# Optimization experiments

Measured on AMD Instinct MI355X. Metric: run time of the kernel, lower is better.

## Reference

```python
import jax, jax.numpy as jnp
import numpy as np

N, E, F, H, EA = 50000, 500000, 2000, 128, 2
NUM_BOND_TYPES = 100
COORDS_RANGE = 10.0
NORM_FACTOR = 100.0


def setup_inputs() -> dict:
    key = jax.random.key(0)
    ks = jax.random.split(key, 20)

    def lin(k, i, o, gain=1.0):
        # xavier-uniform-ish init, stored as [in, out] so forward is x @ W + b
        lim = gain * np.sqrt(6.0 / (i + o))
        return jax.random.uniform(k, (i, o), jnp.float32, -lim, lim)

    inp = {
        "h_a": jax.random.normal(ks[0], (N, H), jnp.float32),
        "x_a": jax.random.normal(ks[1], (N, 3), jnp.float32),
        "e_a_idx": jax.random.randint(ks[2], (2, E), 0, N),
        "e_a_type": jax.random.randint(ks[3], (E,), 0, NUM_BOND_TYPES),
        "e_a_attr": jax.random.normal(ks[4], (E, EA), jnp.float32),
        "coord_diff_a": jax.random.normal(ks[5], (E, 3), jnp.float32),
        "h_f": jax.random.normal(ks[6], (F, H), jnp.float32),
        "x_f": jax.random.normal(ks[7], (F, 3), jnp.float32),
        "bm_mat": jax.random.normal(ks[8], (N, F), jnp.float32) / np.sqrt(F),
        # parameters
        "bond_emb": jax.random.normal(ks[9], (NUM_BOND_TYPES, H), jnp.float32),
        "aW1": lin(ks[10], 2 * H + EA + H, H), "ab1": jnp.zeros((H,), jnp.float32),
        "aW2": lin(ks[11], H, H), "ab2": jnp.zeros((H,), jnp.float32),
        "aW3": lin(ks[12], H, 1, gain=0.001),  # xavier gain=0.001, no bias
        "fW1": lin(ks[13], 2 * H + EA, H), "fb1": jnp.zeros((H,), jnp.float32),
        "fW2": lin(ks[14], H, H), "fb2": jnp.zeros((H,), jnp.float32),
        "fW3": lin(ks[15], H, 1, gain=0.001),
    }
    return inp


def reference(h_a, x_a, e_a_idx, e_a_type, e_a_attr, coord_diff_a, h_f, x_f, bm_mat,
              bond_emb, aW1, ab1, aW2, ab2, aW3, fW1, fb1, fW2, fb2, fW3):
    silu = jax.nn.silu
    row, col = e_a_idx[0], e_a_idx[1]

    be = bond_emb[e_a_type]                              # [E, H]
    coord_diff_f = x_a - bm_mat @ x_f                    # [N, 3]
    radial_f = jnp.sum(coord_diff_f ** 2, axis=1, keepdims=True)  # [N, 1]
    norm_f = jnp.sqrt(radial_f + 1e-8)
    coord_diff_f = coord_diff_f / (norm_f + 1.0)

    inp_atom = jnp.concatenate([h_a[row], h_a[col], e_a_attr, be], axis=1)        # [E, 3H+2]
    inp_frag = jnp.concatenate([h_a, bm_mat @ h_f, radial_f, radial_f], axis=1)   # [N, 2H+2]

    m_atom = silu(silu(inp_atom @ aW1 + ab1) @ aW2 + ab2) @ aW3  # [E, 1]
    m_frag = silu(silu(inp_frag @ fW1 + fb1) @ fW2 + fb2) @ fW3  # [N, 1]

    trans_atom = coord_diff_a * jnp.tanh(m_atom) * COORDS_RANGE  # [E, 3]
    trans_frag = coord_diff_f * jnp.tanh(m_frag) * COORDS_RANGE  # [N, 3]

    agg_atom = jax.ops.segment_sum(trans_atom, row, num_segments=x_a.shape[0]) / NORM_FACTOR
    return x_a + agg_atom + trans_frag
```

## Files before the change

kernel.cpp:

```cpp
#include <hip/hip_runtime.h>
#include <hip/hip_bf16.h>


typedef __attribute__((ext_vector_type(8))) short bfrag8;
typedef __attribute__((ext_vector_type(16))) float f32x16;
typedef __attribute__((ext_vector_type(4))) float f32x4v;

#define MFMA32(A, B, C) __builtin_amdgcn_mfma_f32_32x32x16_bf16((A), (B), (C), 0, 0, 0)

__device__ __forceinline__ f32x16 zero16() {
  f32x16 v;
#pragma unroll
  for (int i = 0; i < 16; ++i) v[i] = 0.0f;
  return v;
}

__device__ __forceinline__ unsigned short bf16bits(float x) {
  __hip_bfloat16 b = __float2bfloat16(x);
  unsigned short u;
  __builtin_memcpy(&u, &b, 2);
  return u;
}

__device__ __forceinline__ unsigned pk2(float lo, float hi) {
  return (unsigned)bf16bits(lo) | ((unsigned)bf16bits(hi) << 16);
}

__device__ __forceinline__ bfrag8 ldfrag(const unsigned short* p) {
  return *reinterpret_cast<const bfrag8*>(p);
}

__device__ __forceinline__ bfrag8 frag4(unsigned f0, unsigned f1, unsigned f2, unsigned f3) {
  union { unsigned u[4]; bfrag8 v; } q;
  q.u[0] = f0; q.u[1] = f1; q.u[2] = f2; q.u[3] = f3;
  return q.v;
}

__device__ __forceinline__ float silu_f(float x) { return x / (1.0f + __expf(-x)); }


__global__ void cvt_bf16_kernel(const float* __restrict__ src, unsigned short* __restrict__ dst, int n4) {
  int t = blockIdx.x * blockDim.x + threadIdx.x;
  if (t < n4) {
    f32x4v v = *reinterpret_cast<const f32x4v*>(src + 4 * (size_t)t);
    unsigned* d = reinterpret_cast<unsigned*>(dst + 4 * (size_t)t);
    d[0] = pk2(v[0], v[1]);
    d[1] = pk2(v[2], v[3]);
  }
}

__global__ void hfp_kernel(const float* __restrict__ h_f, const float* __restrict__ fW1,
                           float* __restrict__ hfp) {
  int f = blockIdx.x, n = threadIdx.x;
  float acc = 0.0f;
  for (int k = 0; k < 128; ++k) acc += h_f[(size_t)f * 128 + k] * fW1[(size_t)(128 + k) * 128 + n];
  hfp[(size_t)f * 128 + n] = acc;
}

__global__ void pack_wT_kernel(const float* __restrict__ W, unsigned short* __restrict__ dst,
                               int kcCount, int Krows) {
  int t = blockIdx.x * blockDim.x + threadIdx.x;
  int total = kcCount * 4 * 64 * 8;
  if (t >= total) return;
  int j = t & 7, l = (t >> 3) & 63, rem = t >> 9;
  int nt = rem & 3, kc = rem >> 2;
  int k = kc * 16 + ((l >> 5) << 3) + j;
  int n = nt * 32 + (l & 31);
  float v = (k < Krows) ? W[(size_t)k * 128 + n] : 0.0f;
  dst[t] = bf16bits(v);
}

__global__ void pack_w1e_kernel(const float* __restrict__ aW1, const float* __restrict__ ab1,
                                unsigned short* __restrict__ dst) {
  int t = blockIdx.x * blockDim.x + threadIdx.x;
  if (t >= 4 * 64 * 8) return;
  int j = t & 7, l = (t >> 3) & 63, nt = (t >> 9) & 3;
  int k = ((l >> 5) << 3) + j;
  int n = nt * 32 + (l & 31);
  float v = (k == 0) ? aW1[(size_t)256 * 128 + n]
          : (k == 1) ? aW1[(size_t)257 * 128 + n]
          : (k == 2) ? ab1[n] : 0.0f;
  dst[t] = bf16bits(v);
}

__global__ void pack_bmat_kernel(const float* __restrict__ hfp, const float* __restrict__ x_f,
                                 unsigned short* __restrict__ dst, int total) {
  int t = blockIdx.x * blockDim.x + threadIdx.x;
  if (t >= total) return;
  int j = t & 7, l = (t >> 3) & 63, rem = t >> 9;
  int nt = rem % 5, kc = rem / 5;
  int k = kc * 16 + ((l >> 5) << 3) + j;
  int n = nt * 32 + (l & 31);
  float v;
  if (n < 128) v = hfp[(size_t)k * 128 + n];
  else if (n < 131) v = x_f[(size_t)k * 3 + (n - 128)];
  else v = 0.0f;
  dst[t] = bf16bits(v);
}

__global__ __launch_bounds__(64) void k1_bm_gemm(
    const float* __restrict__ bm, const unsigned short* __restrict__ bmT,
    float* __restrict__ outT, int N, int F) {
  const int lane = threadIdx.x;
  const int h = lane >> 5;
  const int ln = lane & 31;
  const int m = blockIdx.x * 32 + ln;
  const int mc = (m < N) ? m : (N - 1);
  const float* bp = bm + (size_t)mc * F + h * 8;
  const int KC = F >> 4;

  f32x16 acc[5];
#pragma unroll
  for (int i = 0; i < 5; ++i) acc[i] = zero16();

  f32x4v x0 = *reinterpret_cast<const f32x4v*>(bp);
  f32x4v x1 = *reinterpret_cast<const f32x4v*>(bp + 4);
  for (int kc = 0; kc < KC; ++kc) {
    f32x4v c0 = x0, c1 = x1;
    if (kc + 1 < KC) {
      x0 = *reinterpret_cast<const f32x4v*>(bp + (size_t)(kc + 1) * 16);
      x1 = *reinterpret_cast<const f32x4v*>(bp + (size_t)(kc + 1) * 16 + 4);
    }
    bfrag8 b = frag4(pk2(c0[0], c0[1]), pk2(c0[2], c0[3]), pk2(c1[0], c1[1]), pk2(c1[2], c1[3]));
    const unsigned short* wp = bmT + ((size_t)kc * 5 * 64 + lane) * 8;
#pragma unroll
    for (int nt = 0; nt < 5; ++nt) acc[nt] = MFMA32(ldfrag(wp + nt * 512), b, acc[nt]);
  }
  if (m < N) {
#pragma unroll
    for (int nt = 0; nt < 5; ++nt)
#pragma unroll
      for (int r = 0; r < 16; ++r) {
        int n = nt * 32 + (r & 3) + 8 * (r >> 2) + 4 * h;
        if (n < 131) outT[(size_t)n * N + m] = acc[nt][r];
      }
  }
}

__global__ __launch_bounds__(256) void k2_frag(
    const float* __restrict__ x_a, const unsigned short* __restrict__ h_bf,
    const float* __restrict__ k1T,
    const unsigned short* __restrict__ fW1aT, const unsigned short* __restrict__ fW2T,
    const float* __restrict__ fW1, const float* __restrict__ fb1,
    const float* __restrict__ fb2, const float* __restrict__ fW3,
    float* __restrict__ out, int N) {
  const int lane = threadIdx.x & 63;
  const int wid = threadIdx.x >> 6;
  const int h = lane >> 5;
  const int ln = lane & 31;
  const int i = blockIdx.x * 128 + wid * 32 + ln;
  const bool valid = (i < N);
  const int ic = valid ? i : (N - 1);

  float cd[3];
  float radial = 0.0f;
#pragma unroll
  for (int c = 0; c < 3; ++c) {
    float v = x_a[3 * (size_t)ic + c] - k1T[(size_t)(128 + c) * N + ic];
    cd[c] = v;
    radial += v * v;
  }

  f32x16 acc[4];
#pragma unroll
  for (int q = 0; q < 4; ++q) acc[q] = zero16();
  const unsigned short* hp = h_bf + (size_t)ic * 128 + h * 8;
#pragma unroll
  for (int kc = 0; kc < 8; ++kc) {
    bfrag8 b = ldfrag(hp + kc * 16);
    const unsigned short* wp = fW1aT + ((size_t)(kc * 4) * 64 + lane) * 8;
#pragma unroll
    for (int nt = 0; nt < 4; ++nt) acc[nt] = MFMA32(ldfrag(wp + nt * 512), b, acc[nt]);
  }

  unsigned w[4][8];
#pragma unroll
  for (int nt = 0; nt < 4; ++nt)
#pragma unroll
    for (int p = 0; p < 8; ++p) {
      const int r0 = 2 * p;
      const int n0 = nt * 32 + (r0 & 3) + 8 * (r0 >> 2) + 4 * h;
      const int n1 = n0 + 1;
      float q0 = acc[nt][r0] + k1T[(size_t)n0 * N + ic]
               + radial * (fW1[(size_t)256 * 128 + n0] + fW1[(size_t)257 * 128 + n0]) + fb1[n0];
      float q1 = acc[nt][r0 + 1] + k1T[(size_t)n1 * N + ic]
               + radial * (fW1[(size_t)256 * 128 + n1] + fW1[(size_t)257 * 128 + n1]) + fb1[n1];
      w[nt][p] = pk2(silu_f(q0), silu_f(q1));
    }

  f32x16 acc2[4];
#pragma unroll
  for (int q = 0; q < 4; ++q) acc2[q] = zero16();
#pragma unroll
  for (int kc = 0; kc < 8; ++kc) {
    const int nt1 = kc >> 1, o = (kc & 1) * 4;
    unsigned a0 = w[nt1][o + 0], a1 = w[nt1][o + 1], a2 = w[nt1][o + 2], a3 = w[nt1][o + 3];
    unsigned s0 = (unsigned)__shfl_xor((int)a0, 32);
    unsigned s1 = (unsigned)__shfl_xor((int)a1, 32);
    unsigned s2 = (unsigned)__shfl_xor((int)a2, 32);
    unsigned s3 = (unsigned)__shfl_xor((int)a3, 32);
    bfrag8 b = frag4(h ? s2 : a0, h ? s3 : a1, h ? a2 : s0, h ? a3 : s1);
    const unsigned short* wp = fW2T + ((size_t)(kc * 4) * 64 + lane) * 8;
#pragma unroll
    for (int nt = 0; nt < 4; ++nt) acc2[nt] = MFMA32(ldfrag(wp + nt * 512), b, acc2[nt]);
  }

  float part = 0.0f;
#pragma unroll
  for (int nt = 0; nt < 4; ++nt)
#pragma unroll
    for (int r = 0; r < 16; ++r) {
      int n = nt * 32 + (r & 3) + 8 * (r >> 2) + 4 * h;
      part += silu_f(acc2[nt][r] + fb2[n]) * fW3[n];
    }
  float mv = part + __shfl_xor(part, 32);

  if (valid && h == 0) {
    float nrm = sqrtf(radial + 1e-8f);
    float s = tanhf(mv) * 10.0f / (nrm + 1.0f);
#pragma unroll
    for (int c = 0; c < 3; ++c)
      out[3 * (size_t)i + c] = x_a[3 * (size_t)i + c] + cd[c] * s;
  }
}

__global__ __launch_bounds__(256) void k3_atom(
    const unsigned short* __restrict__ h_bf,
    const unsigned short* __restrict__ bond_bf,
    const int* __restrict__ eidx, const int* __restrict__ etype,
    const float* __restrict__ eattr, const float* __restrict__ cda,
    const unsigned short* __restrict__ W1aT, const unsigned short* __restrict__ W1bT,
    const unsigned short* __restrict__ W1cT, const unsigned short* __restrict__ W1eT,
    const unsigned short* __restrict__ W2T,
    const float* __restrict__ ab2, const float* __restrict__ aW3,
    float* __restrict__ out, int E) {
  const int lane = threadIdx.x & 63;
  const int wid = threadIdx.x >> 6;
  const int h = lane >> 5;
  const int ln = lane & 31;
  const int e = blockIdx.x * 128 + wid * 32 + ln;
  const bool valid = (e < E);
  const int ec = valid ? e : (E - 1);
  const int row = eidx[ec];
  const int col = eidx[(size_t)E + ec];
  const int typ = etype[ec];
  const float e0 = eattr[2 * (size_t)ec];
  const float e1 = eattr[2 * (size_t)ec + 1];

  const unsigned short* hr = h_bf + (size_t)row * 128 + h * 8;
  const unsigned short* hc = h_bf + (size_t)col * 128 + h * 8;
  const unsigned short* bb = bond_bf + (size_t)typ * 128 + h * 8;

  f32x16 acc[4];
#pragma unroll
  for (int q = 0; q < 4; ++q) acc[q] = zero16();

#pragma unroll
  for (int kc = 0; kc < 8; ++kc) {
    bfrag8 b = ldfrag(hr + kc * 16);
    const unsigned short* wp = W1aT + ((size_t)(kc * 4) * 64 + lane) * 8;
#pragma unroll
    for (int nt = 0; nt < 4; ++nt) acc[nt] = MFMA32(ldfrag(wp + nt * 512), b, acc[nt]);
  }
#pragma unroll
  for (int kc = 0; kc < 8; ++kc) {
    bfrag8 b = ldfrag(hc + kc * 16);
    const unsigned short* wp = W1bT + ((size_t)(kc * 4) * 64 + lane) * 8;
#pragma unroll
    for (int nt = 0; nt < 4; ++nt) acc[nt] = MFMA32(ldfrag(wp + nt * 512), b, acc[nt]);
  }
#pragma unroll
  for (int kc = 0; kc < 8; ++kc) {
    bfrag8 b = ldfrag(bb + kc * 16);
    const unsigned short* wp = W1cT + ((size_t)(kc * 4) * 64 + lane) * 8;
#pragma unroll
    for (int nt = 0; nt < 4; ++nt) acc[nt] = MFMA32(ldfrag(wp + nt * 512), b, acc[nt]);
  }
  {
    unsigned u0 = h ? 0u : pk2(e0, e1);
    unsigned u1 = h ? 0u : 0x00003F80u;
    bfrag8 b = frag4(u0, u1, 0u, 0u);
    const unsigned short* wp = W1eT + (size_t)lane * 8;
#pragma unroll
    for (int nt = 0; nt < 4; ++nt) acc[nt] = MFMA32(ldfrag(wp + nt * 512), b, acc[nt]);
  }

  unsigned w[4][8];
#pragma unroll
  for (int nt = 0; nt < 4; ++nt)
#pragma unroll
    for (int p = 0; p < 8; ++p)
      w[nt][p] = pk2(silu_f(acc[nt][2 * p]), silu_f(acc[nt][2 * p + 1]));

  f32x16 acc2[4];
#pragma unroll
  for (int q = 0; q < 4; ++q) acc2[q] = zero16();
#pragma unroll
  for (int kc = 0; kc < 8; ++kc) {
    const int nt1 = kc >> 1, o = (kc & 1) * 4;
    unsigned a0 = w[nt1][o + 0], a1 = w[nt1][o + 1], a2 = w[nt1][o + 2], a3 = w[nt1][o + 3];
    unsigned s0 = (unsigned)__shfl_xor((int)a0, 32);
    unsigned s1 = (unsigned)__shfl_xor((int)a1, 32);
    unsigned s2 = (unsigned)__shfl_xor((int)a2, 32);
    unsigned s3 = (unsigned)__shfl_xor((int)a3, 32);
    bfrag8 b = frag4(h ? s2 : a0, h ? s3 : a1, h ? a2 : s0, h ? a3 : s1);
    const unsigned short* wp = W2T + ((size_t)(kc * 4) * 64 + lane) * 8;
#pragma unroll
    for (int nt = 0; nt < 4; ++nt) acc2[nt] = MFMA32(ldfrag(wp + nt * 512), b, acc2[nt]);
  }

  float part = 0.0f;
#pragma unroll
  for (int nt = 0; nt < 4; ++nt)
#pragma unroll
    for (int r = 0; r < 16; ++r) {
      int n = nt * 32 + (r & 3) + 8 * (r >> 2) + 4 * h;
      part += silu_f(acc2[nt][r] + ab2[n]) * aW3[n];
    }
  float mv = part + __shfl_xor(part, 32);

  if (valid) {
    float t = tanhf(mv) * 0.1f;
    if (h == 0) {
      atomicAdd(out + 3 * (size_t)row + 0, cda[3 * (size_t)ec + 0] * t);
      atomicAdd(out + 3 * (size_t)row + 1, cda[3 * (size_t)ec + 1] * t);
    } else {
      atomicAdd(out + 3 * (size_t)row + 2, cda[3 * (size_t)ec + 2] * t);
    }
  }
}


extern "C" void kernel_launch(void* const* d_in, const int* in_sizes, int n_in,
                              void* d_out, int out_size, void* d_ws, size_t ws_size,
                              hipStream_t stream) {
  const float* h_a    = (const float*)d_in[0];
  const float* x_a    = (const float*)d_in[1];
  const int*   e_idx  = (const int*)d_in[2];
  const int*   e_type = (const int*)d_in[3];
  const float* e_attr = (const float*)d_in[4];
  const float* cda    = (const float*)d_in[5];
  const float* h_f    = (const float*)d_in[6];
  const float* x_f    = (const float*)d_in[7];
  const float* bm     = (const float*)d_in[8];
  const float* bond   = (const float*)d_in[9];
  const float* aW1    = (const float*)d_in[10];
  const float* ab1    = (const float*)d_in[11];
  const float* aW2    = (const float*)d_in[12];
  const float* ab2    = (const float*)d_in[13];
  const float* aW3    = (const float*)d_in[14];
  const float* fW1    = (const float*)d_in[15];
  const float* fb1    = (const float*)d_in[16];
  const float* fW2    = (const float*)d_in[17];
  const float* fb2    = (const float*)d_in[18];
  const float* fW3    = (const float*)d_in[19];
  float* out = (float*)d_out;

  const int N  = in_sizes[0] / 128;
  const int E  = in_sizes[2] / 2;
  const int F  = in_sizes[6] / 128;
  const int NB = in_sizes[9] / 128;
  const int KC = F / 16;

  char* wsp = (char*)d_ws;
  size_t off = 0;
  auto alloc = [&](size_t bytes) -> char* {
    char* p = wsp + off;
    off += (bytes + 255) & ~(size_t)255;
    return p;
  };
  unsigned short* h_bf    = (unsigned short*)alloc((size_t)N * 128 * 2);
  unsigned short* bond_bf = (unsigned short*)alloc((size_t)NB * 128 * 2);
  float*          hfp     = (float*)alloc((size_t)F * 128 * 4);
  unsigned short* bmT     = (unsigned short*)alloc((size_t)KC * 5 * 64 * 8 * 2);
  unsigned short* W1aT    = (unsigned short*)alloc(8 * 4 * 64 * 8 * 2);
  unsigned short* W1bT    = (unsigned short*)alloc(8 * 4 * 64 * 8 * 2);
  unsigned short* W1cT    = (unsigned short*)alloc(8 * 4 * 64 * 8 * 2);
  unsigned short* W2T     = (unsigned short*)alloc(8 * 4 * 64 * 8 * 2);
  unsigned short* fW1aT   = (unsigned short*)alloc(8 * 4 * 64 * 8 * 2);
  unsigned short* fW2T    = (unsigned short*)alloc(8 * 4 * 64 * 8 * 2);
  unsigned short* W1eT    = (unsigned short*)alloc(1 * 4 * 64 * 8 * 2);
  float*          k1T     = (float*)alloc((size_t)131 * N * 4);

  {
    int n4 = N * 128 / 4;
    cvt_bf16_kernel<<<(n4 + 255) / 256, 256, 0, stream>>>(h_a, h_bf, n4);
  }
  {
    int n4 = NB * 128 / 4;
    cvt_bf16_kernel<<<(n4 + 255) / 256, 256, 0, stream>>>(bond, bond_bf, n4);
  }
  hfp_kernel<<<F, 128, 0, stream>>>(h_f, fW1, hfp);
  {
    int total = KC * 5 * 64 * 8;
    pack_bmat_kernel<<<(total + 255) / 256, 256, 0, stream>>>(hfp, x_f, bmT, total);
  }
  pack_wT_kernel<<<64, 256, 0, stream>>>(aW1,                 W1aT, 8, 128);
  pack_wT_kernel<<<64, 256, 0, stream>>>(aW1 + 128 * 128,     W1bT, 8, 128);
  pack_wT_kernel<<<64, 256, 0, stream>>>(aW1 + 258 * 128,     W1cT, 8, 128);
  pack_wT_kernel<<<64, 256, 0, stream>>>(aW2,                 W2T,  8, 128);
  pack_wT_kernel<<<64, 256, 0, stream>>>(fW1,                 fW1aT, 8, 128);
  pack_wT_kernel<<<64, 256, 0, stream>>>(fW2,                 fW2T, 8, 128);
  pack_w1e_kernel<<<8, 256, 0, stream>>>(aW1, ab1, W1eT);

  k1_bm_gemm<<<(N + 31) / 32, 64, 0, stream>>>(bm, bmT, k1T, N, F);
  k2_frag<<<(N + 127) / 128, 256, 0, stream>>>(x_a, h_bf, k1T, fW1aT, fW2T,
                                               fW1, fb1, fb2, fW3, out, N);
  k3_atom<<<(E + 127) / 128, 256, 0, stream>>>(h_bf, bond_bf, e_idx, e_type, e_attr, cda,
                                               W1aT, W1bT, W1cT, W1eT, W2T, ab2, aW3, out, E);
}
```

Before: 384.1 us.

## Merge prep kernels and run bm GEMM alongside edge MLP in one launch

Folds the bf16 conversion, hfp matmul, weight packing and aggregation-buffer zeroing into a single block-partitioned prep kernel. The bm GEMM and edge MLP now run as one grid, so the long-K GEMM blocks can overlap with edge blocks instead of running serially. Edge atomics now target a separate agg buffer that the node kernel adds into the output. The h_bf layout is changed so each half-wave reads 64 contiguous elements, and the GEMM uses 4-wave blocks with a two-stage prefetch. Costs are an extra N×3 buffer and launch bounds (256,2) that may limit registers for the edge path.

```diff
diff --git a/kernel.cpp b/kernel.cpp
--- a/kernel.cpp
+++ b/kernel.cpp
@@ -38,49 +38,101 @@
 
 __device__ __forceinline__ float silu_f(float x) { return x / (1.0f + __expf(-x)); }
 
-
-__global__ void cvt_bf16_kernel(const float* __restrict__ src, unsigned short* __restrict__ dst, int n4) {
-  int t = blockIdx.x * blockDim.x + threadIdx.x;
-  if (t < n4) {
-    f32x4v v = *reinterpret_cast<const f32x4v*>(src + 4 * (size_t)t);
-    unsigned* d = reinterpret_cast<unsigned*>(dst + 4 * (size_t)t);
-    d[0] = pk2(v[0], v[1]);
-    d[1] = pk2(v[2], v[3]);
-  }
-}
-
-__global__ void hfp_kernel(const float* __restrict__ h_f, const float* __restrict__ fW1,
-                           float* __restrict__ hfp) {
-  int f = blockIdx.x, n = threadIdx.x;
-  float acc = 0.0f;
-  for (int k = 0; k < 128; ++k) acc += h_f[(size_t)f * 128 + k] * fW1[(size_t)(128 + k) * 128 + n];
-  hfp[(size_t)f * 128 + n] = acc;
-}
-
-__global__ void pack_wT_kernel(const float* __restrict__ W, unsigned short* __restrict__ dst,
-                               int kcCount, int Krows) {
-  int t = blockIdx.x * blockDim.x + threadIdx.x;
-  int total = kcCount * 4 * 64 * 8;
-  if (t >= total) return;
-  int j = t & 7, l = (t >> 3) & 63, rem = t >> 9;
-  int nt = rem & 3, kc = rem >> 2;
-  int k = kc * 16 + ((l >> 5) << 3) + j;
-  int n = nt * 32 + (l & 31);
-  float v = (k < Krows) ? W[(size_t)k * 128 + n] : 0.0f;
-  dst[t] = bf16bits(v);
-}
-
-__global__ void pack_w1e_kernel(const float* __restrict__ aW1, const float* __restrict__ ab1,
-                                unsigned short* __restrict__ dst) {
-  int t = blockIdx.x * blockDim.x + threadIdx.x;
-  if (t >= 4 * 64 * 8) return;
-  int j = t & 7, l = (t >> 3) & 63, nt = (t >> 9) & 3;
-  int k = ((l >> 5) << 3) + j;
-  int n = nt * 32 + (l & 31);
-  float v = (k == 0) ? aW1[(size_t)256 * 128 + n]
-          : (k == 1) ? aW1[(size_t)257 * 128 + n]
-          : (k == 2) ? ab1[n] : 0.0f;
-  dst[t] = bf16bits(v);
+__global__ __launch_bounds__(256) void prep_kernel(
+    const float* __restrict__ h_a, const float* __restrict__ bond,
+    const float* __restrict__ h_f,
+    const float* __restrict__ aW1, const float* __restrict__ ab1,
+    const float* __restrict__ aW2,
+    const float* __restrict__ fW1, const float* __restrict__ fW2,
+    unsigned short* __restrict__ h_bf, unsigned short* __restrict__ bond_bf,
+    float* __restrict__ hfp,
+    unsigned short* __restrict__ W1aT, unsigned short* __restrict__ W1bT,
+    unsigned short* __restrict__ W1cT, unsigned short* __restrict__ W1eT,
+    unsigned short* __restrict__ W2T,
+    unsigned short* __restrict__ fW1aT, unsigned short* __restrict__ fW2T,
+    float* __restrict__ agg,
+    int N, int NB, int F) {
+  const int t = threadIdx.x;
+  int bid = blockIdx.x;
+  const int G_A = (N * 16 + 255) >> 8;
+  const int G_B = (NB * 16 + 255) >> 8;
+  const int G_H = (F + 1) >> 1;
+
+  if (bid < G_A + G_B) {
+    const float* src = (bid < G_A) ? h_a : bond;
+    unsigned short* dst = (bid < G_A) ? h_bf : bond_bf;
+    int rows = (bid < G_A) ? N : NB;
+    int idx = (bid < G_A ? bid : bid - G_A) * 256 + t;
+    if (idx < rows * 16) {
+      int row = idx >> 4, g = idx & 15;
+      int h = g & 1, kc = g >> 1;
+      const f32x4v* s = reinterpret_cast<const f32x4v*>(src + (size_t)row * 128 + g * 8);
+      f32x4v v0 = s[0], v1 = s[1];
+      unsigned* d = reinterpret_cast<unsigned*>(dst + (size_t)row * 128 + h * 64 + kc * 8);
+      d[0] = pk2(v0[0], v0[1]);
+      d[1] = pk2(v0[2], v0[3]);
+      d[2] = pk2(v1[0], v1[1]);
+      d[3] = pk2(v1[2], v1[3]);
+    }
+    return;
+  }
+  bid -= G_A + G_B;
+  if (bid < G_H) {
+    int f = bid * 2 + (t >> 7), n = t & 127;
+    if (f < F) {
+      float acc = 0.0f;
+#pragma unroll 8
+      for (int k = 0; k < 128; ++k)
+        acc += h_f[(size_t)f * 128 + k] * fW1[(size_t)(128 + k) * 128 + n];
+      hfp[(size_t)f * 128 + n] = acc;
+    }
+    return;
+  }
+  bid -= G_H;
+  if (bid < 6 * 64) {
+    int p = bid >> 6;
+    int tt = (bid & 63) * 256 + t;
+    int j = tt & 7, l = (tt >> 3) & 63, rem = tt >> 9;
+    int nt = rem & 3, kc = rem >> 2;
+    int k = kc * 16 + ((l >> 5) << 3) + j;
+    int n = nt * 32 + (l & 31);
+    const float* W;
+    unsigned short* D;
+    switch (p) {
+      case 0: W = aW1;             D = W1aT;  break;
+      case 1: W = aW1 + 128 * 128; D = W1bT;  break;
+      case 2: W = aW1 + 258 * 128; D = W1cT;  break;
+      case 3: W = aW2;             D = W2T;   break;
+      case 4: W = fW1;             D = fW1aT; break;
+      default: W = fW2;            D = fW2T;  break;
+    }
+    D[tt] = bf16bits(W[(size_t)k * 128 + n]);
+    return;
+  }
+  bid -= 6 * 64;
+  if (bid < 8) {
+    int tt = bid * 256 + t;
+    if (tt < 4 * 64 * 8) {
+      int j = tt & 7, l = (tt >> 3) & 63, nt = (tt >> 9) & 3;
+      int k = ((l >> 5) << 3) + j;
+      int n = nt * 32 + (l & 31);
+      float v = (k == 0) ? aW1[(size_t)256 * 128 + n]
+              : (k == 1) ? aW1[(size_t)257 * 128 + n]
+              : (k == 2) ? ab1[n] : 0.0f;
+      W1eT[tt] = bf16bits(v);
+    }
+    return;
+  }
+  bid -= 8;
+  {
+    int i4 = (bid * 256 + t) * 4;
+    if (i4 + 3 < N * 3) {
+      *reinterpret_cast<f32x4v*>(agg + i4) = f32x4v{0.f, 0.f, 0.f, 0.f};
+    } else {
+      for (int c = 0; c < 4; ++c)
+        if (i4 + c < N * 3) agg[i4 + c] = 0.0f;
+    }
+  }
 }
 
 __global__ void pack_bmat_kernel(const float* __restrict__ hfp, const float* __restrict__ x_f,
@@ -98,48 +150,155 @@
   dst[t] = bf16bits(v);
 }
 
-__global__ __launch_bounds__(64) void k1_bm_gemm(
+__global__ __launch_bounds__(256, 2) void fused_k1_k3(
     const float* __restrict__ bm, const unsigned short* __restrict__ bmT,
-    float* __restrict__ outT, int N, int F) {
-  const int lane = threadIdx.x;
+    float* __restrict__ k1T,
+    const unsigned short* __restrict__ h_bf, const unsigned short* __restrict__ bond_bf,
+    const int* __restrict__ eidx, const int* __restrict__ etype,
+    const float* __restrict__ eattr, const float* __restrict__ cda,
+    const unsigned short* __restrict__ W1aT, const unsigned short* __restrict__ W1bT,
+    const unsigned short* __restrict__ W1cT, const unsigned short* __restrict__ W1eT,
+    const unsigned short* __restrict__ W2T,
+    const float* __restrict__ ab2, const float* __restrict__ aW3,
+    float* __restrict__ agg,
+    int N, int F, int E, int G1) {
+  const int lane = threadIdx.x & 63;
+  const int wid = threadIdx.x >> 6;
   const int h = lane >> 5;
   const int ln = lane & 31;
-  const int m = blockIdx.x * 32 + ln;
-  const int mc = (m < N) ? m : (N - 1);
-  const float* bp = bm + (size_t)mc * F + h * 8;
-  const int KC = F >> 4;
-
-  f32x16 acc[5];
-#pragma unroll
-  for (int i = 0; i < 5; ++i) acc[i] = zero16();
-
-  f32x4v x0 = *reinterpret_cast<const f32x4v*>(bp);
-  f32x4v x1 = *reinterpret_cast<const f32x4v*>(bp + 4);
-  for (int kc = 0; kc < KC; ++kc) {
-    f32x4v c0 = x0, c1 = x1;
-    if (kc + 1 < KC) {
-      x0 = *reinterpret_cast<const f32x4v*>(bp + (size_t)(kc + 1) * 16);
-      x1 = *reinterpret_cast<const f32x4v*>(bp + (size_t)(kc + 1) * 16 + 4);
-    }
-    bfrag8 b = frag4(pk2(c0[0], c0[1]), pk2(c0[2], c0[3]), pk2(c1[0], c1[1]), pk2(c1[2], c1[3]));
-    const unsigned short* wp = bmT + ((size_t)kc * 5 * 64 + lane) * 8;
-#pragma unroll
-    for (int nt = 0; nt < 5; ++nt) acc[nt] = MFMA32(ldfrag(wp + nt * 512), b, acc[nt]);
-  }
-  if (m < N) {
-#pragma unroll
-    for (int nt = 0; nt < 5; ++nt)
-#pragma unroll
-      for (int r = 0; r < 16; ++r) {
-        int n = nt * 32 + (r & 3) + 8 * (r >> 2) + 4 * h;
-        if (n < 131) outT[(size_t)n * N + m] = acc[nt][r];
+
+  if ((int)blockIdx.x < G1) {
+    const int m = blockIdx.x * 128 + wid * 32 + ln;
+    const int mc = (m < N) ? m : (N - 1);
+    const float* bp = bm + (size_t)mc * F + h * 8;
+    const int KC = F >> 4;
+
+    f32x16 acc[5];
+#pragma unroll
+    for (int i = 0; i < 5; ++i) acc[i] = zero16();
+
+    f32x4v a0 = *reinterpret_cast<const f32x4v*>(bp);
+    f32x4v a1 = *reinterpret_cast<const f32x4v*>(bp + 4);
+    f32x4v b0 = *reinterpret_cast<const f32x4v*>(bp + 16);
+    f32x4v b1 = *reinterpret_cast<const f32x4v*>(bp + 20);
+    for (int kc = 0; kc < KC; ++kc) {
+      f32x4v c0 = a0, c1 = a1;
+      a0 = b0; a1 = b1;
+      if (kc + 2 < KC) {
+        b0 = *reinterpret_cast<const f32x4v*>(bp + (size_t)(kc + 2) * 16);
+        b1 = *reinterpret_cast<const f32x4v*>(bp + (size_t)(kc + 2) * 16 + 4);
       }
+      bfrag8 b = frag4(pk2(c0[0], c0[1]), pk2(c0[2], c0[3]), pk2(c1[0], c1[1]), pk2(c1[2], c1[3]));
+      const unsigned short* wp = bmT + ((size_t)kc * 5 * 64 + lane) * 8;
+#pragma unroll
+      for (int nt = 0; nt < 5; ++nt) acc[nt] = MFMA32(ldfrag(wp + nt * 512), b, acc[nt]);
+    }
+    if (m < N) {
+#pragma unroll
+      for (int nt = 0; nt < 5; ++nt)
+#pragma unroll
+        for (int r = 0; r < 16; ++r) {
+          int n = nt * 32 + (r & 3) + 8 * (r >> 2) + 4 * h;
+          if (n < 131) k1T[(size_t)n * N + m] = acc[nt][r];
+        }
+    }
+    return;
+  }
+
+  const int e = (blockIdx.x - G1) * 128 + wid * 32 + ln;
+  const bool valid = (e < E);
+  const int ec = valid ? e : (E - 1);
+  const int row = eidx[ec];
+  const int col = eidx[(size_t)E + ec];
+  const int typ = etype[ec];
+  const float e0 = eattr[2 * (size_t)ec];
+  const float e1 = eattr[2 * (size_t)ec + 1];
+
+  const unsigned short* hr = h_bf + (size_t)row * 128 + h * 64;
+  const unsigned short* hc = h_bf + (size_t)col * 128 + h * 64;
+  const unsigned short* bb = bond_bf + (size_t)typ * 128 + h * 64;
+
+  f32x16 acc[4];
+#pragma unroll
+  for (int q = 0; q < 4; ++q) acc[q] = zero16();
+
+#pragma unroll
+  for (int kc = 0; kc < 8; ++kc) {
+    bfrag8 b = ldfrag(hr + kc * 8);
+    const unsigned short* wp = W1aT + ((size_t)(kc * 4) * 64 + lane) * 8;
+#pragma unroll
+    for (int nt = 0; nt < 4; ++nt) acc[nt] = MFMA32(ldfrag(wp + nt * 512), b, acc[nt]);
+  }
+#pragma unroll
+  for (int kc = 0; kc < 8; ++kc) {
+    bfrag8 b = ldfrag(hc + kc * 8);
+    const unsigned short* wp = W1bT + ((size_t)(kc * 4) * 64 + lane) * 8;
+#pragma unroll
+    for (int nt = 0; nt < 4; ++nt) acc[nt] = MFMA32(ldfrag(wp + nt * 512), b, acc[nt]);
+  }
+#pragma unroll
+  for (int kc = 0; kc < 8; ++kc) {
+    bfrag8 b = ldfrag(bb + kc * 8);
+    const unsigned short* wp = W1cT + ((size_t)(kc * 4) * 64 + lane) * 8;
+#pragma unroll
+    for (int nt = 0; nt < 4; ++nt) acc[nt] = MFMA32(ldfrag(wp + nt * 512), b, acc[nt]);
+  }
+  {
+    unsigned u0 = h ? 0u : pk2(e0, e1);
+    unsigned u1 = h ? 0u : 0x00003F80u;
+    bfrag8 b = frag4(u0, u1, 0u, 0u);
+    const unsigned short* wp = W1eT + (size_t)lane * 8;
+#pragma unroll
+    for (int nt = 0; nt < 4; ++nt) acc[nt] = MFMA32(ldfrag(wp + nt * 512), b, acc[nt]);
+  }
+
+  unsigned w[32];
+#pragma unroll
+  for (int nt = 0; nt < 4; ++nt)
+#pragma unroll
+    for (int p = 0; p < 8; ++p)
+      w[nt * 8 + p] = pk2(silu_f(acc[nt][2 * p]), silu_f(acc[nt][2 * p + 1]));
+
+#pragma unroll
+  for (int q = 0; q < 4; ++q) acc[q] = zero16();
+#pragma unroll
+  for (int kc = 0; kc < 8; ++kc) {
+    const int base = (kc >> 1) * 8 + (kc & 1) * 4;
+    unsigned a0 = w[base + 0], a1 = w[base + 1], a2 = w[base + 2], a3 = w[base + 3];
+    unsigned s0 = (unsigned)__shfl_xor((int)a0, 32);
+    unsigned s1 = (unsigned)__shfl_xor((int)a1, 32);
+    unsigned s2 = (unsigned)__shfl_xor((int)a2, 32);
+    unsigned s3 = (unsigned)__shfl_xor((int)a3, 32);
+    bfrag8 b = frag4(h ? s2 : a0, h ? s3 : a1, h ? a2 : s0, h ? a3 : s1);
+    const unsigned short* wp = W2T + ((size_t)(kc * 4) * 64 + lane) * 8;
+#pragma unroll
+    for (int nt = 0; nt < 4; ++nt) acc[nt] = MFMA32(ldfrag(wp + nt * 512), b, acc[nt]);
+  }
+
+  float part = 0.0f;
+#pragma unroll
+  for (int nt = 0; nt < 4; ++nt)
+#pragma unroll
+    for (int r = 0; r < 16; ++r) {
+      int n = nt * 32 + (r & 3) + 8 * (r >> 2) + 4 * h;
+      part += silu_f(acc[nt][r] + ab2[n]) * aW3[n];
+    }
+  float mv = part + __shfl_xor(part, 32);
+
+  if (valid) {
+    float t = tanhf(mv) * 0.1f;
+    if (h == 0) {
+      atomicAdd(agg + 3 * (size_t)row + 0, cda[3 * (size_t)ec + 0] * t);
+      atomicAdd(agg + 3 * (size_t)row + 1, cda[3 * (size_t)ec + 1] * t);
+    } else {
+      atomicAdd(agg + 3 * (size_t)row + 2, cda[3 * (size_t)ec + 2] * t);
+    }
   }
 }
 
 __global__ __launch_bounds__(256) void k2_frag(
     const float* __restrict__ x_a, const unsigned short* __restrict__ h_bf,
-    const float* __restrict__ k1T,
+    const float* __restrict__ k1T, const float* __restrict__ agg,
     const unsigned short* __restrict__ fW1aT, const unsigned short* __restrict__ fW2T,
     const float* __restrict__ fW1, const float* __restrict__ fb1,
     const float* __restrict__ fb2, const float* __restrict__ fW3,
@@ -164,16 +323,16 @@
   f32x16 acc[4];
 #pragma unroll
   for (int q = 0; q < 4; ++q) acc[q] = zero16();
-  const unsigned short* hp = h_bf + (size_t)ic * 128 + h * 8;
-#pragma unroll
-  for (int kc = 0; kc < 8; ++kc) {
-    bfrag8 b = ldfrag(hp + kc * 16);
+  const unsigned short* hp = h_bf + (size_t)ic * 128 + h * 64;
+#pragma unroll
+  for (int kc = 0; kc < 8; ++kc) {
+    bfrag8 b = ldfrag(hp + kc * 8);
     const unsigned short* wp = fW1aT + ((size_t)(kc * 4) * 64 + lane) * 8;
 #pragma unroll
     for (int nt = 0; nt < 4; ++nt) acc[nt] = MFMA32(ldfrag(wp + nt * 512), b, acc[nt]);
   }
 
-  unsigned w[4][8];
+  unsigned w[32];
 #pragma unroll
   for (int nt = 0; nt < 4; ++nt)
 #pragma unroll
@@ -185,16 +344,15 @@
                + radial * (fW1[(size_t)256 * 128 + n0] + fW1[(size_t)257 * 128 + n0]) + fb1[n0];
       float q1 = acc[nt][r0 + 1] + k1T[(size_t)n1 * N + ic]
                + radial * (fW1[(size_t)256 * 128 + n1] + fW1[(size_t)257 * 128 + n1]) + fb1[n1];
-      w[nt][p] = pk2(silu_f(q0), silu_f(q1));
-    }
-
-  f32x16 acc2[4];
-#pragma unroll
-  for (int q = 0; q < 4; ++q) acc2[q] = zero16();
-#pragma unroll
-  for (int kc = 0; kc < 8; ++kc) {
-    const int nt1 = kc >> 1, o = (kc & 1) * 4;
-    unsigned a0 = w[nt1][o + 0], a1 = w[nt1][o + 1], a2 = w[nt1][o + 2], a3 = w[nt1][o + 3];
+      w[nt * 8 + p] = pk2(silu_f(q0), silu_f(q1));
+    }
+
+#pragma unroll
+  for (int q = 0; q < 4; ++q) acc[q] = zero16();
+#pragma unroll
+  for (int kc = 0; kc < 8; ++kc) {
+    const int base = (kc >> 1) * 8 + (kc & 1) * 4;
+    unsigned a0 = w[base + 0], a1 = w[base + 1], a2 = w[base + 2], a3 = w[base + 3];
     unsigned s0 = (unsigned)__shfl_xor((int)a0, 32);
     unsigned s1 = (unsigned)__shfl_xor((int)a1, 32);
     unsigned s2 = (unsigned)__shfl_xor((int)a2, 32);
@@ -202,7 +360,7 @@
     bfrag8 b = frag4(h ? s2 : a0, h ? s3 : a1, h ? a2 : s0, h ? a3 : s1);
     const unsigned short* wp = fW2T + ((size_t)(kc * 4) * 64 + lane) * 8;
 #pragma unroll
-    for (int nt = 0; nt < 4; ++nt) acc2[nt] = MFMA32(ldfrag(wp + nt * 512), b, acc2[nt]);
+    for (int nt = 0; nt < 4; ++nt) acc[nt] = MFMA32(ldfrag(wp + nt * 512), b, acc[nt]);
   }
 
   float part = 0.0f;
@@ -211,7 +369,7 @@
 #pragma unroll
     for (int r = 0; r < 16; ++r) {
       int n = nt * 32 + (r & 3) + 8 * (r >> 2) + 4 * h;
-      part += silu_f(acc2[nt][r] + fb2[n]) * fW3[n];
+      part += silu_f(acc[nt][r] + fb2[n]) * fW3[n];
     }
   float mv = part + __shfl_xor(part, 32);
 
@@ -220,113 +378,7 @@
     float s = tanhf(mv) * 10.0f / (nrm + 1.0f);
 #pragma unroll
     for (int c = 0; c < 3; ++c)
-      out[3 * (size_t)i + c] = x_a[3 * (size_t)i + c] + cd[c] * s;
-  }
-}
-
-__global__ __launch_bounds__(256) void k3_atom(
-    const unsigned short* __restrict__ h_bf,
-    const unsigned short* __restrict__ bond_bf,
-    const int* __restrict__ eidx, const int* __restrict__ etype,
-    const float* __restrict__ eattr, const float* __restrict__ cda,
-    const unsigned short* __restrict__ W1aT, const unsigned short* __restrict__ W1bT,
-    const unsigned short* __restrict__ W1cT, const unsigned short* __restrict__ W1eT,
-    const unsigned short* __restrict__ W2T,
-    const float* __restrict__ ab2, const float* __restrict__ aW3,
-    float* __restrict__ out, int E) {
-  const int lane = threadIdx.x & 63;
-  const int wid = threadIdx.x >> 6;
-  const int h = lane >> 5;
-  const int ln = lane & 31;
-  const int e = blockIdx.x * 128 + wid * 32 + ln;
-  const bool valid = (e < E);
-  const int ec = valid ? e : (E - 1);
-  const int row = eidx[ec];
-  const int col = eidx[(size_t)E + ec];
-  const int typ = etype[ec];
-  const float e0 = eattr[2 * (size_t)ec];
-  const float e1 = eattr[2 * (size_t)ec + 1];
-
-  const unsigned short* hr = h_bf + (size_t)row * 128 + h * 8;
-  const unsigned short* hc = h_bf + (size_t)col * 128 + h * 8;
-  const unsigned short* bb = bond_bf + (size_t)typ * 128 + h * 8;
-
-  f32x16 acc[4];
-#pragma unroll
-  for (int q = 0; q < 4; ++q) acc[q] = zero16();
-
-#pragma unroll
-  for (int kc = 0; kc < 8; ++kc) {
-    bfrag8 b = ldfrag(hr + kc * 16);
-    const unsigned short* wp = W1aT + ((size_t)(kc * 4) * 64 + lane) * 8;
-#pragma unroll
-    for (int nt = 0; nt < 4; ++nt) acc[nt] = MFMA32(ldfrag(wp + nt * 512), b, acc[nt]);
-  }
-#pragma unroll
-  for (int kc = 0; kc < 8; ++kc) {
-    bfrag8 b = ldfrag(hc + kc * 16);
-    const unsigned short* wp = W1bT + ((size_t)(kc * 4) * 64 + lane) * 8;
-#pragma unroll
-    for (int nt = 0; nt < 4; ++nt) acc[nt] = MFMA32(ldfrag(wp + nt * 512), b, acc[nt]);
-  }
-#pragma unroll
-  for (int kc = 0; kc < 8; ++kc) {
-    bfrag8 b = ldfrag(bb + kc * 16);
-    const unsigned short* wp = W1cT + ((size_t)(kc * 4) * 64 + lane) * 8;
-#pragma unroll
-    for (int nt = 0; nt < 4; ++nt) acc[nt] = MFMA32(ldfrag(wp + nt * 512), b, acc[nt]);
-  }
-  {
-    unsigned u0 = h ? 0u : pk2(e0, e1);
-    unsigned u1 = h ? 0u : 0x00003F80u;
-    bfrag8 b = frag4(u0, u1, 0u, 0u);
-    const unsigned short* wp = W1eT + (size_t)lane * 8;
-#pragma unroll
-    for (int nt = 0; nt < 4; ++nt) acc[nt] = MFMA32(ldfrag(wp + nt * 512), b, acc[nt]);
-  }
-
-  unsigned w[4][8];
-#pragma unroll
-  for (int nt = 0; nt < 4; ++nt)
-#pragma unroll
-    for (int p = 0; p < 8; ++p)
-      w[nt][p] = pk2(silu_f(acc[nt][2 * p]), silu_f(acc[nt][2 * p + 1]));
-
-  f32x16 acc2[4];
-#pragma unroll
-  for (int q = 0; q < 4; ++q) acc2[q] = zero16();
-#pragma unroll
-  for (int kc = 0; kc < 8; ++kc) {
-    const int nt1 = kc >> 1, o = (kc & 1) * 4;
-    unsigned a0 = w[nt1][o + 0], a1 = w[nt1][o + 1], a2 = w[nt1][o + 2], a3 = w[nt1][o + 3];
-    unsigned s0 = (unsigned)__shfl_xor((int)a0, 32);
-    unsigned s1 = (unsigned)__shfl_xor((int)a1, 32);
-    unsigned s2 = (unsigned)__shfl_xor((int)a2, 32);
-    unsigned s3 = (unsigned)__shfl_xor((int)a3, 32);
-    bfrag8 b = frag4(h ? s2 : a0, h ? s3 : a1, h ? a2 : s0, h ? a3 : s1);
-    const unsigned short* wp = W2T + ((size_t)(kc * 4) * 64 + lane) * 8;
-#pragma unroll
-    for (int nt = 0; nt < 4; ++nt) acc2[nt] = MFMA32(ldfrag(wp + nt * 512), b, acc2[nt]);
-  }
-
-  float part = 0.0f;
-#pragma unroll
-  for (int nt = 0; nt < 4; ++nt)
-#pragma unroll
-    for (int r = 0; r < 16; ++r) {
-      int n = nt * 32 + (r & 3) + 8 * (r >> 2) + 4 * h;
-      part += silu_f(acc2[nt][r] + ab2[n]) * aW3[n];
-    }
-  float mv = part + __shfl_xor(part, 32);
-
-  if (valid) {
-    float t = tanhf(mv) * 0.1f;
-    if (h == 0) {
-      atomicAdd(out + 3 * (size_t)row + 0, cda[3 * (size_t)ec + 0] * t);
-      atomicAdd(out + 3 * (size_t)row + 1, cda[3 * (size_t)ec + 1] * t);
-    } else {
-      atomicAdd(out + 3 * (size_t)row + 2, cda[3 * (size_t)ec + 2] * t);
-    }
+      out[3 * (size_t)i + c] = x_a[3 * (size_t)i + c] + cd[c] * s + agg[3 * (size_t)i + c];
   }
 }
 
@@ -381,31 +433,32 @@
   unsigned short* fW2T    = (unsigned short*)alloc(8 * 4 * 64 * 8 * 2);
   unsigned short* W1eT    = (unsigned short*)alloc(1 * 4 * 64 * 8 * 2);
   float*          k1T     = (float*)alloc((size_t)131 * N * 4);
-
-  {
-    int n4 = N * 128 / 4;
-    cvt_bf16_kernel<<<(n4 + 255) / 256, 256, 0, stream>>>(h_a, h_bf, n4);
-  }
-  {
-    int n4 = NB * 128 / 4;
-    cvt_bf16_kernel<<<(n4 + 255) / 256, 256, 0, stream>>>(bond, bond_bf, n4);
-  }
-  hfp_kernel<<<F, 128, 0, stream>>>(h_f, fW1, hfp);
+  float*          agg     = (float*)alloc((size_t)N * 3 * 4);
+
+  const int G_A = (N * 16 + 255) >> 8;
+  const int G_B = (NB * 16 + 255) >> 8;
+  const int G_H = (F + 1) >> 1;
+  const int G_P = 6 * 64;
+  const int G_E2 = 8;
+  const int G_Z = (N * 3 + 1023) >> 10;
+  prep_kernel<<<G_A + G_B + G_H + G_P + G_E2 + G_Z, 256, 0, stream>>>(
+      h_a, bond, h_f, aW1, ab1, aW2, fW1, fW2,
+      h_bf, bond_bf, hfp, W1aT, W1bT, W1cT, W1eT, W2T, fW1aT, fW2T, agg,
+      N, NB, F);
+
   {
     int total = KC * 5 * 64 * 8;
     pack_bmat_kernel<<<(total + 255) / 256, 256, 0, stream>>>(hfp, x_f, bmT, total);
   }
-  pack_wT_kernel<<<64, 256, 0, stream>>>(aW1,                 W1aT, 8, 128);
-  pack_wT_kernel<<<64, 256, 0, stream>>>(aW1 + 128 * 128,     W1bT, 8, 128);
-  pack_wT_kernel<<<64, 256, 0, stream>>>(aW1 + 258 * 128,     W1cT, 8, 128);
-  pack_wT_kernel<<<64, 256, 0, stream>>>(aW2,                 W2T,  8, 128);
-  pack_wT_kernel<<<64, 256, 0, stream>>>(fW1,                 fW1aT, 8, 128);
-  pack_wT_kernel<<<64, 256, 0, stream>>>(fW2,                 fW2T, 8, 128);
-  pack_w1e_kernel<<<8, 256, 0, stream>>>(aW1, ab1, W1eT);
-
-  k1_bm_gemm<<<(N + 31) / 32, 64, 0, stream>>>(bm, bmT, k1T, N, F);
-  k2_frag<<<(N + 127) / 128, 256, 0, stream>>>(x_a, h_bf, k1T, fW1aT, fW2T,
+
+  const int G1 = (N + 127) / 128;
+  const int G3 = (E + 127) / 128;
+  fused_k1_k3<<<G1 + G3, 256, 0, stream>>>(
+      bm, bmT, k1T,
+      h_bf, bond_bf, e_idx, e_type, e_attr, cda,
+      W1aT, W1bT, W1cT, W1eT, W2T, ab2, aW3, agg,
+      N, F, E, G1);
+
+  k2_frag<<<(N + 127) / 128, 256, 0, stream>>>(x_a, h_bf, k1T, agg, fW1aT, fW2T,
                                                fW1, fb1, fb2, fW3, out, N);
-  k3_atom<<<(E + 127) / 128, 256, 0, stream>>>(h_bf, bond_bf, e_idx, e_type, e_attr, cda,
-                                               W1aT, W1bT, W1cT, W1eT, W2T, ab2, aW3, out, E);
-}
+}
```

Measured after the change: 381.2 us. No clear change (-0.8%).
